# Optimization experiments

Hardware: AMD Instinct MI355X
Metric: run time of the kernel (lower is better)

The kernel has to match this reference:

```python
import jax, jax.numpy as jnp
import numpy as np

B, N, K = 128, 131072, 256


def setup_inputs() -> dict:
    key = jax.random.key(0)
    k1, k2 = jax.random.split(key)
    score = jax.random.normal(k1, (B, N), dtype=jnp.float32)
    roi = jax.random.uniform(k2, (B, N, 4), dtype=jnp.float32)
    return {"score": score, "roi": roi, "k": K}


def reference(score, roi, k):
    # top-k over the anchor dim, sorted descending (matches tf.nn.top_k sorted=True)
    top_k_score, top_k_index = jax.lax.top_k(score, k)  # [B, k], [B, k]
    # gather ROI rows: equivalent of tf.gather_nd with (batch_idx, anchor_idx)
    roi_selected = jnp.take_along_axis(roi, top_k_index[:, :, None], axis=1)  # [B, k, 4]
    return roi_selected, top_k_score
```

## Files before the change

### kernel.cpp

```cpp
#include <hip/hip_runtime.h>
#include <stdint.h>


#define BATCH   128
#define NANCH   131072
#define KSEL    256
#define SPLITS  8
#define CHUNK   (NANCH / SPLITS)
#define TPB     256
#define V4PT    (CHUNK / TPB / 4)
#define NBUCK   4096
#define CAPMAX  8192
#define SORTCAP 2048

typedef unsigned long long ull;

__device__ __forceinline__ unsigned ord_of(float f) {
    unsigned u = __float_as_uint(f);
    return (u & 0x80000000u) ? ~u : (u | 0x80000000u);
}
__device__ __forceinline__ float f_of_ord(unsigned o) {
    unsigned u = (o & 0x80000000u) ? (o ^ 0x80000000u) : ~o;
    return __uint_as_float(u);
}

__global__ __launch_bounds__(TPB) void topk_stage1(
    const float* __restrict__ score, ull* __restrict__ cand,
    int* __restrict__ cnt, int cap)
{
    __shared__ int hist[NBUCK];
    __shared__ int scan[TPB];
    __shared__ int s_bstar;
    __shared__ int s_base;

    const int t  = threadIdx.x;
    const int sp = blockIdx.x;
    const int b  = blockIdx.y;

    const float4* src = (const float4*)(score + (size_t)b * NANCH + (size_t)sp * CHUNK);
    float4 v[V4PT];
#pragma unroll
    for (int i = 0; i < V4PT; ++i) v[i] = src[i * TPB + t];

    for (int i = t; i < NBUCK; i += TPB) hist[i] = 0;
    __syncthreads();

#pragma unroll
    for (int i = 0; i < V4PT; ++i) {
        atomicAdd(&hist[ord_of(v[i].x) >> 20], 1);
        atomicAdd(&hist[ord_of(v[i].y) >> 20], 1);
        atomicAdd(&hist[ord_of(v[i].z) >> 20], 1);
        atomicAdd(&hist[ord_of(v[i].w) >> 20], 1);
    }
    __syncthreads();

    int ps = 0;
#pragma unroll
    for (int p = 0; p < 16; ++p) ps += hist[t * 16 + p];
    scan[t] = ps;
    __syncthreads();
    for (int off = 1; off < TPB; off <<= 1) {
        int add = (t + off < TPB) ? scan[t + off] : 0;
        __syncthreads();
        scan[t] += add;
        __syncthreads();
    }
    {
        int running = (t + 1 < TPB) ? scan[t + 1] : 0;
#pragma unroll
        for (int p = 15; p >= 0; --p) {
            int nr = running + hist[t * 16 + p];
            if (nr >= KSEL && running < KSEL) s_bstar = t * 16 + p;
            running = nr;
        }
    }
    __syncthreads();
    const unsigned thr = (unsigned)s_bstar << 20;

    int qc = 0;
#pragma unroll
    for (int i = 0; i < V4PT; ++i) {
        qc += (ord_of(v[i].x) >= thr);
        qc += (ord_of(v[i].y) >= thr);
        qc += (ord_of(v[i].z) >= thr);
        qc += (ord_of(v[i].w) >= thr);
    }
    __syncthreads();
    scan[t] = qc;
    __syncthreads();
    for (int off = 1; off < TPB; off <<= 1) {
        int add = (t >= off) ? scan[t - off] : 0;
        __syncthreads();
        scan[t] += add;
        __syncthreads();
    }
    if (t == TPB - 1) s_base = atomicAdd(&cnt[b], scan[TPB - 1]);
    __syncthreads();

    int pos = s_base + scan[t] - qc;
    ull* cb = cand + (size_t)b * cap;
    const int nbase = sp * CHUNK;
#pragma unroll
    for (int i = 0; i < V4PT; ++i) {
        const int n0 = nbase + 4 * (i * TPB + t);
        unsigned o;
        o = ord_of(v[i].x);
        if (o >= thr && pos < cap) { cb[pos++] = ((ull)o << 32) | (unsigned)(NANCH - 1 - n0); }
        o = ord_of(v[i].y);
        if (o >= thr && pos < cap) { cb[pos++] = ((ull)o << 32) | (unsigned)(NANCH - 2 - n0); }
        o = ord_of(v[i].z);
        if (o >= thr && pos < cap) { cb[pos++] = ((ull)o << 32) | (unsigned)(NANCH - 3 - n0); }
        o = ord_of(v[i].w);
        if (o >= thr && pos < cap) { cb[pos++] = ((ull)o << 32) | (unsigned)(NANCH - 4 - n0); }
    }
}

__global__ __launch_bounds__(TPB) void topk_stage2(
    const ull* __restrict__ cand, const int* __restrict__ cnt,
    const float* __restrict__ roi, float* __restrict__ out_roi,
    float* __restrict__ out_score, int cap)
{
    __shared__ int hist[NBUCK];
    __shared__ int scan[TPB];
    __shared__ ull buf[SORTCAP];
    __shared__ int s_bstar, s_csel;

    const int t = threadIdx.x;
    const int b = blockIdx.x;
    const int c = min(cnt[b], cap);
    const ull* cb = cand + (size_t)b * cap;

    for (int i = t; i < NBUCK; i += TPB) hist[i] = 0;
    if (t == 0) s_csel = 0;
    __syncthreads();
    for (int i = t; i < c; i += TPB) atomicAdd(&hist[(unsigned)(cb[i] >> 52)], 1);
    __syncthreads();

    int ps = 0;
#pragma unroll
    for (int p = 0; p < 16; ++p) ps += hist[t * 16 + p];
    scan[t] = ps;
    __syncthreads();
    for (int off = 1; off < TPB; off <<= 1) {
        int add = (t + off < TPB) ? scan[t + off] : 0;
        __syncthreads();
        scan[t] += add;
        __syncthreads();
    }
    {
        int running = (t + 1 < TPB) ? scan[t + 1] : 0;
#pragma unroll
        for (int p = 15; p >= 0; --p) {
            int nr = running + hist[t * 16 + p];
            if (nr >= KSEL && running < KSEL) s_bstar = t * 16 + p;
            running = nr;
        }
    }
    __syncthreads();
    const unsigned bstar = (unsigned)s_bstar;

    for (int i = t; i < c; i += TPB) {
        ull k = cb[i];
        if ((unsigned)(k >> 52) >= bstar) {
            int p = atomicAdd(&s_csel, 1);
            if (p < SORTCAP) buf[p] = k;
        }
    }
    __syncthreads();
    const int C = min(s_csel, SORTCAP);
    int P = KSEL;
    while (P < C) P <<= 1;
    for (int i = C + t; i < P; i += TPB) buf[i] = 0;
    __syncthreads();

    for (int kk = 2; kk <= P; kk <<= 1) {
        for (int j = kk >> 1; j > 0; j >>= 1) {
            for (int i = t; i < P; i += TPB) {
                int ixj = i ^ j;
                if (ixj > i) {
                    ull a = buf[i], d = buf[ixj];
                    bool up = (i & kk) == 0;
                    bool sw = up ? (a < d) : (a > d);
                    if (sw) { buf[i] = d; buf[ixj] = a; }
                }
            }
            __syncthreads();
        }
    }

    ull k = buf[t];
    unsigned o = (unsigned)(k >> 32);
    int idx = NANCH - 1 - (int)(unsigned)(k & 0xffffffffull);
    out_score[b * KSEL + t] = f_of_ord(o);
    float4 r = ((const float4*)roi)[(size_t)b * NANCH + idx];
    ((float4*)out_roi)[b * KSEL + t] = r;
}

extern "C" void kernel_launch(void* const* d_in, const int* in_sizes, int n_in,
                              void* d_out, int out_size, void* d_ws, size_t ws_size,
                              hipStream_t stream)
{
    const float* score = (const float*)d_in[0];
    const float* roi   = (const float*)d_in[1];
    float* out_roi   = (float*)d_out;
    float* out_score = (float*)d_out + (size_t)BATCH * KSEL * 4;

    int* cnt  = (int*)d_ws;
    ull* cand = (ull*)((char*)d_ws + 4096);
    long long avail = ((long long)ws_size - 4096) / (long long)(sizeof(ull) * BATCH);
    int cap = (int)avail;
    if (cap > CAPMAX) cap = CAPMAX;
    if (cap < 1) cap = 1;

    hipMemsetAsync(cnt, 0, BATCH * sizeof(int), stream);
    topk_stage1<<<dim3(SPLITS, BATCH), TPB, 0, stream>>>(score, cand, cnt, cap);
    topk_stage2<<<BATCH, TPB, 0, stream>>>(cand, cnt, roi, out_roi, out_score, cap);
}
```

Baseline: 369.2 us.

## Replace block LDS histogram threshold with per-wave binary-search radix select

In stage 1, each 64-lane wavefront now finds its own top-256 threshold with a 12-step binary search over the upper bucket bits. Each step counts matches in registers and sums them with a wave shuffle, replacing the shared-memory atomic histogram and the block-wide scans with their many __syncthreads. Candidate compaction also uses a wave-level shuffle scan with one global atomic per wave. Because every wave keeps at least 256 candidates, the per-batch candidate buffer grows to a fixed 24576 entries, which adds stage-2 read and histogram work. The workspace-size check is removed, so there is a risk of overrunning a workspace that is too small.

```diff
diff --git a/kernel.cpp b/kernel.cpp
--- a/kernel.cpp
+++ b/kernel.cpp
@@ -8,15 +8,13 @@
 #define SPLITS  8
 #define CHUNK   (NANCH / SPLITS)
 #define TPB     256
-#define V4PT    (CHUNK / TPB / 4)
 #define NBUCK   4096
-#define CAPMAX  8192
+#define CAP     24576
 #define SORTCAP 2048
 
 typedef unsigned long long ull;
 
-__device__ __forceinline__ unsigned ord_of(float f) {
-    unsigned u = __float_as_uint(f);
+__device__ __forceinline__ unsigned ord_of_bits(unsigned u) {
     return (u & 0x80000000u) ? ~u : (u | 0x80000000u);
 }
 __device__ __forceinline__ float f_of_ord(unsigned o) {
@@ -24,101 +22,82 @@
     return __uint_as_float(u);
 }
 
-__global__ __launch_bounds__(TPB) void topk_stage1(
+__global__ __launch_bounds__(TPB, 4) void topk_stage1(
     const float* __restrict__ score, ull* __restrict__ cand,
-    int* __restrict__ cnt, int cap)
+    int* __restrict__ cnt)
 {
-    __shared__ int hist[NBUCK];
-    __shared__ int scan[TPB];
-    __shared__ int s_bstar;
-    __shared__ int s_base;
+    const int t    = threadIdx.x;
+    const int lane = t & 63;
+    const int w    = t >> 6;
+    const int sp   = blockIdx.x;
+    const int b    = blockIdx.y;
 
-    const int t  = threadIdx.x;
-    const int sp = blockIdx.x;
-    const int b  = blockIdx.y;
+    const uint4* src = (const uint4*)(score + (size_t)b * NANCH + (size_t)sp * CHUNK)
+                       + w * 1024 + lane;
+    uint4 u[16];
+#pragma unroll
+    for (int i = 0; i < 16; ++i) u[i] = src[i * 64];
+#pragma unroll
+    for (int i = 0; i < 16; ++i) {
+        u[i].x = ord_of_bits(u[i].x);
+        u[i].y = ord_of_bits(u[i].y);
+        u[i].z = ord_of_bits(u[i].z);
+        u[i].w = ord_of_bits(u[i].w);
+    }
 
-    const float4* src = (const float4*)(score + (size_t)b * NANCH + (size_t)sp * CHUNK);
-    float4 v[V4PT];
+    int lo = 0, hi = NBUCK - 1;
+    while (lo < hi) {
+        const int mid = (lo + hi + 1) >> 1;
+        const unsigned piv = (unsigned)mid << 20;
+        int c = 0;
 #pragma unroll
-    for (int i = 0; i < V4PT; ++i) v[i] = src[i * TPB + t];
-
-    for (int i = t; i < NBUCK; i += TPB) hist[i] = 0;
-    __syncthreads();
-
+        for (int i = 0; i < 16; ++i) {
+            c += (u[i].x >= piv) + (u[i].y >= piv) + (u[i].z >= piv) + (u[i].w >= piv);
+        }
 #pragma unroll
-    for (int i = 0; i < V4PT; ++i) {
-        atomicAdd(&hist[ord_of(v[i].x) >> 20], 1);
-        atomicAdd(&hist[ord_of(v[i].y) >> 20], 1);
-        atomicAdd(&hist[ord_of(v[i].z) >> 20], 1);
-        atomicAdd(&hist[ord_of(v[i].w) >> 20], 1);
+        for (int s = 1; s < 64; s <<= 1) c += __shfl_xor(c, s);
+        if (c >= KSEL) lo = mid; else hi = mid - 1;
     }
-    __syncthreads();
-
-    int ps = 0;
-#pragma unroll
-    for (int p = 0; p < 16; ++p) ps += hist[t * 16 + p];
-    scan[t] = ps;
-    __syncthreads();
-    for (int off = 1; off < TPB; off <<= 1) {
-        int add = (t + off < TPB) ? scan[t + off] : 0;
-        __syncthreads();
-        scan[t] += add;
-        __syncthreads();
-    }
-    {
-        int running = (t + 1 < TPB) ? scan[t + 1] : 0;
-#pragma unroll
-        for (int p = 15; p >= 0; --p) {
-            int nr = running + hist[t * 16 + p];
-            if (nr >= KSEL && running < KSEL) s_bstar = t * 16 + p;
-            running = nr;
-        }
-    }
-    __syncthreads();
-    const unsigned thr = (unsigned)s_bstar << 20;
+    const unsigned thr = (unsigned)lo << 20;
 
     int qc = 0;
 #pragma unroll
-    for (int i = 0; i < V4PT; ++i) {
-        qc += (ord_of(v[i].x) >= thr);
-        qc += (ord_of(v[i].y) >= thr);
-        qc += (ord_of(v[i].z) >= thr);
-        qc += (ord_of(v[i].w) >= thr);
+    for (int i = 0; i < 16; ++i) {
+        qc += (u[i].x >= thr) + (u[i].y >= thr) + (u[i].z >= thr) + (u[i].w >= thr);
     }
-    __syncthreads();
-    scan[t] = qc;
-    __syncthreads();
-    for (int off = 1; off < TPB; off <<= 1) {
-        int add = (t >= off) ? scan[t - off] : 0;
-        __syncthreads();
-        scan[t] += add;
-        __syncthreads();
+    int incl = qc;
+#pragma unroll
+    for (int s = 1; s < 64; s <<= 1) {
+        int y = __shfl_up(incl, s);
+        if (lane >= s) incl += y;
     }
-    if (t == TPB - 1) s_base = atomicAdd(&cnt[b], scan[TPB - 1]);
-    __syncthreads();
+    const int tot = __shfl(incl, 63);
+    int gbase = 0;
+    if (lane == 0) gbase = atomicAdd(&cnt[b], tot);
+    gbase = __shfl(gbase, 0);
 
-    int pos = s_base + scan[t] - qc;
-    ull* cb = cand + (size_t)b * cap;
-    const int nbase = sp * CHUNK;
+    ull* cb = cand + (size_t)b * CAP;
+    int pos = gbase + (incl - qc);
+    const int nbase = sp * CHUNK + (w * 1024 + lane) * 4;
 #pragma unroll
-    for (int i = 0; i < V4PT; ++i) {
-        const int n0 = nbase + 4 * (i * TPB + t);
+    for (int i = 0; i < 16; ++i) {
+        const int n0 = nbase + i * 256;
         unsigned o;
-        o = ord_of(v[i].x);
-        if (o >= thr && pos < cap) { cb[pos++] = ((ull)o << 32) | (unsigned)(NANCH - 1 - n0); }
-        o = ord_of(v[i].y);
-        if (o >= thr && pos < cap) { cb[pos++] = ((ull)o << 32) | (unsigned)(NANCH - 2 - n0); }
-        o = ord_of(v[i].z);
-        if (o >= thr && pos < cap) { cb[pos++] = ((ull)o << 32) | (unsigned)(NANCH - 3 - n0); }
-        o = ord_of(v[i].w);
-        if (o >= thr && pos < cap) { cb[pos++] = ((ull)o << 32) | (unsigned)(NANCH - 4 - n0); }
+        o = u[i].x;
+        if (o >= thr && pos < CAP) cb[pos++] = ((ull)o << 32) | (unsigned)(NANCH - 1 - n0);
+        o = u[i].y;
+        if (o >= thr && pos < CAP) cb[pos++] = ((ull)o << 32) | (unsigned)(NANCH - 2 - n0);
+        o = u[i].z;
+        if (o >= thr && pos < CAP) cb[pos++] = ((ull)o << 32) | (unsigned)(NANCH - 3 - n0);
+        o = u[i].w;
+        if (o >= thr && pos < CAP) cb[pos++] = ((ull)o << 32) | (unsigned)(NANCH - 4 - n0);
     }
 }
 
 __global__ __launch_bounds__(TPB) void topk_stage2(
     const ull* __restrict__ cand, const int* __restrict__ cnt,
     const float* __restrict__ roi, float* __restrict__ out_roi,
-    float* __restrict__ out_score, int cap)
+    float* __restrict__ out_score)
 {
     __shared__ int hist[NBUCK];
     __shared__ int scan[TPB];
@@ -127,8 +106,8 @@
 
     const int t = threadIdx.x;
     const int b = blockIdx.x;
-    const int c = min(cnt[b], cap);
-    const ull* cb = cand + (size_t)b * cap;
+    const int c = min(cnt[b], CAP);
+    const ull* cb = cand + (size_t)b * CAP;
 
     for (int i = t; i < NBUCK; i += TPB) hist[i] = 0;
     if (t == 0) s_csel = 0;
@@ -180,8 +159,7 @@
                 if (ixj > i) {
                     ull a = buf[i], d = buf[ixj];
                     bool up = (i & kk) == 0;
-                    bool sw = up ? (a < d) : (a > d);
-                    if (sw) { buf[i] = d; buf[ixj] = a; }
+                    if (up ? (a < d) : (a > d)) { buf[i] = d; buf[ixj] = a; }
                 }
             }
             __syncthreads();
@@ -207,12 +185,8 @@
 
     int* cnt  = (int*)d_ws;
     ull* cand = (ull*)((char*)d_ws + 4096);
-    long long avail = ((long long)ws_size - 4096) / (long long)(sizeof(ull) * BATCH);
-    int cap = (int)avail;
-    if (cap > CAPMAX) cap = CAPMAX;
-    if (cap < 1) cap = 1;
 
     hipMemsetAsync(cnt, 0, BATCH * sizeof(int), stream);
-    topk_stage1<<<dim3(SPLITS, BATCH), TPB, 0, stream>>>(score, cand, cnt, cap);
-    topk_stage2<<<BATCH, TPB, 0, stream>>>(cand, cnt, roi, out_roi, out_score, cap);
+    topk_stage1<<<dim3(SPLITS, BATCH), TPB, 0, stream>>>(score, cand, cnt);
+    topk_stage2<<<BATCH, TPB, 0, stream>>>(cand, cnt, roi, out_roi, out_score);
 }
```

Result: slower. 436.0 us (+18.1%).
